# Optimization experiments

Measured on AMD Instinct MI355X. Metric: run time of the kernel, lower is better.

The kernel has to match this reference:

```python
import jax, jax.numpy as jnp
import numpy as np

H, W = 200, 200           # BEV spatial shape (single level)
NBQ, NH, NL, NP = 2, 8, 1, 4
D = 256
HD = D // NH


def setup_inputs() -> dict:
    key = jax.random.key(0)
    ks = jax.random.split(key, 12)
    bs, nq = 1, H * W
    query = jax.random.normal(ks[0], (bs, nq, D), jnp.float32)
    value = jax.random.normal(ks[1], (bs, NBQ * nq, D), jnp.float32)
    reference_points = jax.random.uniform(ks[2], (bs, nq, NL, 2), dtype=jnp.float32)
    spatial_shapes = jnp.array([[H, W]], dtype=jnp.int32)
    sc = 1.0 / np.sqrt(D)
    W_v = jax.random.normal(ks[3], (D, D), jnp.float32) * sc
    b_v = jax.random.normal(ks[4], (D,), jnp.float32) * 0.01
    W_so = jax.random.normal(ks[5], (2 * D, NBQ * NH * NL * NP * 2), jnp.float32) * 0.02
    b_so = jax.random.normal(ks[6], (NBQ * NH * NL * NP * 2,), jnp.float32) * 0.5
    W_aw = jax.random.normal(ks[7], (2 * D, NBQ * NH * NL * NP), jnp.float32) * 0.02
    b_aw = jax.random.normal(ks[8], (NBQ * NH * NL * NP,), jnp.float32) * 0.01
    W_o = jax.random.normal(ks[9], (D, D), jnp.float32) * sc
    b_o = jax.random.normal(ks[10], (D,), jnp.float32) * 0.01
    return {"query": query, "value": value, "reference_points": reference_points,
            "spatial_shapes": spatial_shapes,
            "W_v": W_v, "b_v": b_v, "W_so": W_so, "b_so": b_so,
            "W_aw": W_aw, "b_aw": b_aw, "W_o": W_o, "b_o": b_o}


def _ms_deform_attn(value, locs, attn):
    # value: (B, K, NH, HD); locs: (B, nq, NH, NL, NP, 2) in [0,1]; attn: (B, nq, NH, NL, NP)
    B, K, h, d = value.shape
    nq = locs.shape[1]
    out = jnp.zeros((B, nq, h, d), value.dtype)
    start = 0
    for l, (Hl, Wl) in enumerate([(H, W)]):
        v = value[:, start:start + Hl * Wl].transpose(0, 2, 1, 3).reshape(B * h, Hl * Wl, d)
        start += Hl * Wl
        g = locs[:, :, :, l]                      # (B, nq, h, NP, 2)
        # grid_sample(align_corners=False, padding='zeros') pixel coords
        x = g[..., 0] * Wl - 0.5
        y = g[..., 1] * Hl - 0.5
        x0 = jnp.floor(x); y0 = jnp.floor(y)
        lx = x - x0; ly = y - y0
        x0 = x0.astype(jnp.int32); y0 = y0.astype(jnp.int32)
        acc = jnp.zeros((B * h, nq * NP, d), value.dtype)
        for dy, wy in ((0, 1.0 - ly), (1, ly)):
            for dx, wx in ((0, 1.0 - lx), (1, lx)):
                xi = x0 + dx; yi = y0 + dy
                valid = ((xi >= 0) & (xi < Wl) & (yi >= 0) & (yi < Hl)).astype(value.dtype)
                idx = jnp.clip(yi, 0, Hl - 1) * Wl + jnp.clip(xi, 0, Wl - 1)  # (B,nq,h,NP)
                idxf = idx.transpose(0, 2, 1, 3).reshape(B * h, nq * NP)
                samp = jnp.take_along_axis(v, idxf[:, :, None], axis=1)       # (B*h, nq*NP, d)
                wgt = (wx * wy * valid).transpose(0, 2, 1, 3).reshape(B * h, nq * NP, 1)
                acc = acc + samp * wgt
        acc = acc.reshape(B, h, nq, NP, d)
        out = out + jnp.einsum('bhqpd,bqhp->bqhd', acc, attn[:, :, :, l])
    return out.reshape(B, nq, h * d)


def reference(query, value, reference_points, spatial_shapes,
              W_v, b_v, W_so, b_so, W_aw, b_aw, W_o, b_o):
    bs, nq, _ = query.shape
    identity = query
    val4 = value.reshape(bs, NBQ, nq, D)
    # query enhanced with most recent bev-queue features
    qe = jnp.concatenate([val4[:, 0], query], axis=-1)           # (bs, nq, 2D)
    vproj = (value @ W_v + b_v).reshape(bs * NBQ, nq, NH, HD)
    off = (qe @ W_so + b_so).reshape(bs, nq, NH, NBQ, NL, NP, 2)
    aw = (qe @ W_aw + b_aw).reshape(bs, nq, NH, NBQ, NL * NP)
    aw = jax.nn.softmax(aw, axis=-1).reshape(bs, nq, NH, NBQ, NL, NP)
    aw = aw.transpose(0, 3, 1, 2, 4, 5).reshape(bs * NBQ, nq, NH, NL, NP)
    # offset normalizer: [W, H] per level
    norm = jnp.stack([spatial_shapes[:, 1], spatial_shapes[:, 0]], -1).astype(query.dtype)  # (NL,2)
    locs = (reference_points[:, :, None, None, :, None, :]
            + off / norm[None, None, None, None, :, None, :])     # (bs,nq,NH,NBQ,NL,NP,2)
    locs = locs.transpose(0, 3, 1, 2, 4, 5, 6).reshape(bs * NBQ, nq, NH, NL, NP, 2)
    out = _ms_deform_attn(vproj, locs, aw)                        # (bs*NBQ, nq, D)
    out = out.reshape(bs, NBQ, nq, D).mean(axis=1)
    return out @ W_o + b_o + identity
```

## Files before the change

kernel.cpp:

```cpp
#include <hip/hip_runtime.h>
#include <math.h>

#define HW_   40000
#define NQ_   40000
#define IMGW  200
#define IMGH  200

typedef __bf16 bf16;
typedef __attribute__((ext_vector_type(4))) __bf16 bf16x4;
typedef __attribute__((ext_vector_type(8))) __bf16 bf16x8;
typedef __attribute__((ext_vector_type(4))) float f32x4;

__device__ __forceinline__ void gload_lds16(const void* g, void* l) {
  __builtin_amdgcn_global_load_lds(
      (const __attribute__((address_space(1))) void*)g,
      (__attribute__((address_space(3))) void*)l, 16, 0, 0);
}

__global__ __launch_bounds__(256) void prep_kernel(
    const float* __restrict__ Wv, const float* __restrict__ Wso,
    const float* __restrict__ Waw, const float* __restrict__ Wo,
    bf16* __restrict__ BtV, bf16* __restrict__ BtOA, bf16* __restrict__ BtO)
{
  int idx = blockIdx.x * 256 + threadIdx.x;
  if (idx < 65536) {
    int k = idx >> 8, n = idx & 255;
    BtV[(size_t)n * 256 + k] = (bf16)Wv[idx];
  } else if (idx < 131072) {
    int j = idx - 65536;
    int k = j >> 7, n = j & 127;
    BtOA[(size_t)n * 512 + k] = (bf16)Wso[j];
  } else if (idx < 163840) {
    int j = idx - 131072;
    int k = j >> 6, n = j & 63;
    BtOA[(size_t)(128 + n) * 512 + k] = (bf16)Waw[j];
  } else if (idx < 229376) {
    int j = idx - 163840;
    int k = j >> 8, n = j & 255;
    BtO[(size_t)n * 256 + k] = (bf16)Wo[j];
  }
}

template<int KT, int MODE, int BN, int AF32>
__global__ __launch_bounds__(256) void mfma_gemm_kernel(
    const void* __restrict__ A0, const void* __restrict__ A1,
    const bf16* __restrict__ Bt,
    const float* __restrict__ bias0, const float* __restrict__ bias1,
    const float* __restrict__ resid,
    void* __restrict__ outp, void* __restrict__ outp2, int M)
{
  constexpr int NT16 = BN / 32;
  constexpr int BCH  = BN / 64;
  __shared__ bf16 As[2][128 * 32];
  __shared__ bf16 Bs[2][BN * 32];
  const int t    = threadIdx.x;
  const int m0   = blockIdx.x * 128;
  const int w    = t >> 6;
  const int lane = t & 63;
  const int quad = lane >> 4;
  const int l16  = lane & 15;
  const int wm   = (w & 1) * 64;
  const int wn   = (w >> 1) * (BN / 2);

  f32x4 acc[4][NT16] = {};

  int gmA[2];
#pragma unroll
  for (int i = 0; i < 2; ++i) {
    int gm = m0 + ((i * 256 + t) >> 2);
    gmA[i] = (gm >= M) ? (M - 1) : gm;
  }

  float4 apf[2][2];

  auto issueB = [&](int it) {
    const int kt  = it * 32;
    const int buf = it & 1;
#pragma unroll
    for (int i = 0; i < BCH; ++i) {
      int c = i * 256 + t;
      gload_lds16(&Bt[(size_t)(c >> 2) * KT + kt + (c & 3) * 8], &Bs[buf][c * 8]);
    }
  };

  auto issueA_lds = [&](int it) {
    const int kt  = it * 32;
    const int buf = it & 1;
    const bf16* Ap;
    int col;
    if (KT == 512) { Ap = (kt < 256) ? (const bf16*)A0 : (const bf16*)A1; col = kt & 255; }
    else           { Ap = (const bf16*)A0; col = kt; }
#pragma unroll
    for (int i = 0; i < 2; ++i) {
      int c = i * 256 + t;
      gload_lds16(&Ap[(size_t)gmA[i] * 256 + col + (c & 3) * 8], &As[buf][c * 8]);
    }
  };

  auto loadA_f32 = [&](int it) {
    const int kt = it * 32;
    const float* Ap;
    int col;
    if (KT == 512) { Ap = (kt < 256) ? (const float*)A0 : (const float*)A1; col = kt & 255; }
    else           { Ap = (const float*)A0; col = kt; }
#pragma unroll
    for (int i = 0; i < 2; ++i) {
      int c = i * 256 + t;
      const float4* s = (const float4*)&Ap[(size_t)gmA[i] * 256 + col + (c & 3) * 8];
      apf[i][0] = s[0];
      apf[i][1] = s[1];
    }
  };

  auto writeA = [&](int it) {
    const int buf = it & 1;
#pragma unroll
    for (int i = 0; i < 2; ++i) {
      int c = i * 256 + t;
      bf16x8 o = {(bf16)apf[i][0].x, (bf16)apf[i][0].y,
                  (bf16)apf[i][0].z, (bf16)apf[i][0].w,
                  (bf16)apf[i][1].x, (bf16)apf[i][1].y,
                  (bf16)apf[i][1].z, (bf16)apf[i][1].w};
      *(bf16x8*)&As[buf][c * 8] = o;
    }
  };

  constexpr int NIT = KT / 32;
  if (AF32) { loadA_f32(0); issueB(0); writeA(0); }
  else      { issueA_lds(0); issueB(0); }

#pragma unroll
  for (int it = 0; it < NIT; ++it) {
    __syncthreads();
    if (it + 1 < NIT) {
      issueB(it + 1);
      if (AF32) loadA_f32(it + 1); else issueA_lds(it + 1);
    }
    const bf16* as = As[it & 1];
    const bf16* bs = Bs[it & 1];
    bf16x8 af[4], bfr[NT16];
#pragma unroll
    for (int x = 0; x < 4; ++x)
      af[x] = *(const bf16x8*)&as[(wm + x * 16 + l16) * 32 + quad * 8];
#pragma unroll
    for (int x = 0; x < NT16; ++x)
      bfr[x] = *(const bf16x8*)&bs[(wn + x * 16 + l16) * 32 + quad * 8];
#pragma unroll
    for (int mt = 0; mt < 4; ++mt)
#pragma unroll
      for (int nt = 0; nt < NT16; ++nt)
        acc[mt][nt] = __builtin_amdgcn_mfma_f32_16x16x32_bf16(
            af[mt], bfr[nt], acc[mt][nt], 0, 0, 0);
    if (AF32 && it + 1 < NIT) writeA(it + 1);
  }

#pragma unroll
  for (int mt = 0; mt < 4; ++mt) {
#pragma unroll
    for (int r = 0; r < 4; ++r) {
      const int gm = m0 + wm + mt * 16 + quad * 4 + r;
      if (gm >= M) continue;
#pragma unroll
      for (int nt = 0; nt < NT16; ++nt) {
        const int gn = wn + nt * 16 + l16;
        float v = acc[mt][nt][r];
        if (MODE == 0) {
          int nbq = (gm >= HW_) ? 1 : 0;
          int pix = gm - nbq * HW_;
          int h = gn >> 5, hd = gn & 31;
          ((bf16*)outp)[(((size_t)(nbq * 8 + h) * HW_ + pix) << 5) + hd] =
              (bf16)(v + bias0[gn]);
        } else if (MODE == 1) {
          if (gn < 128)
            ((bf16*)outp)[(size_t)gm * 128 + gn] = (bf16)(v + bias0[gn]);
          else
            ((bf16*)outp2)[(size_t)gm * 64 + (gn - 128)] =
                (bf16)(v + bias1[gn - 128]);
        } else {
          ((float*)outp)[(size_t)gm * 256 + gn] =
              v + bias0[gn] + resid[(size_t)gm * 256 + gn];
        }
      }
    }
  }
}

__global__ __launch_bounds__(256) void deform_attn_kernel(
    const bf16* __restrict__ vws,
    const bf16* __restrict__ off_bf,
    const bf16* __restrict__ aw_bf,
    const float* __restrict__ ref,
    bf16* __restrict__ ms)
{
  const int t    = threadIdx.x;
  const int w    = t >> 6;
  const int lane = t & 63;
  const int h    = blockIdx.x & 7;
  const int qb   = blockIdx.x >> 3;
  const int qi   = lane >> 3;
  const int q    = qb * 32 + w * 8 + qi;
  const int nbq  = (lane >> 2) & 1;
  const int sub  = lane & 3;
  const int g    = h * 2 + nbq;

  const float rx = ref[2 * q + 0] * (float)IMGW - 0.5f;
  const float ry = ref[2 * q + 1] * (float)IMGH - 0.5f;

  bf16x4 a4 = *(const bf16x4*)&aw_bf[(size_t)q * 64 + g * 4];
  float aa0 = (float)a4[0], aa1 = (float)a4[1], aa2 = (float)a4[2], aa3 = (float)a4[3];
  float mx = fmaxf(fmaxf(aa0, aa1), fmaxf(aa2, aa3));
  float e0 = __expf(aa0 - mx), e1 = __expf(aa1 - mx);
  float e2 = __expf(aa2 - mx), e3 = __expf(aa3 - mx);
  float inv = 1.0f / (e0 + e1 + e2 + e3);
  float w4[4] = {e0 * inv, e1 * inv, e2 * inv, e3 * inv};

  bf16x8 o8 = *(const bf16x8*)&off_bf[(size_t)q * 128 + g * 8];
  float ox[4] = {(float)o8[0], (float)o8[2], (float)o8[4], (float)o8[6]};
  float oy[4] = {(float)o8[1], (float)o8[3], (float)o8[5], (float)o8[7]};

  const bf16* vbase = vws + (((size_t)(nbq * 8 + h) * HW_) << 5) + sub * 8;

  float acc[8] = {};
#pragma unroll
  for (int p = 0; p < 4; ++p) {
    float x = rx + ox[p];
    float y = ry + oy[p];
    float xf = floorf(x), yf = floorf(y);
    int   x0 = (int)xf,   y0 = (int)yf;
    float lx = x - xf,    ly = y - yf;
    int   x1 = x0 + 1,    y1 = y0 + 1;
    float w00 = (1.0f - lx) * (1.0f - ly);
    float w01 = lx * (1.0f - ly);
    float w10 = (1.0f - lx) * ly;
    float w11 = lx * ly;
    if (x0 < 0 || x0 >= IMGW) { w00 = 0.0f; w10 = 0.0f; }
    if (x1 < 0 || x1 >= IMGW) { w01 = 0.0f; w11 = 0.0f; }
    if (y0 < 0 || y0 >= IMGH) { w00 = 0.0f; w01 = 0.0f; }
    if (y1 < 0 || y1 >= IMGH) { w10 = 0.0f; w11 = 0.0f; }
    int xc0 = min(max(x0, 0), IMGW - 1), xc1 = min(max(x1, 0), IMGW - 1);
    int yc0 = min(max(y0, 0), IMGH - 1), yc1 = min(max(y1, 0), IMGH - 1);
    bf16x8 v00 = *(const bf16x8*)&vbase[(size_t)(yc0 * IMGW + xc0) << 5];
    bf16x8 v01 = *(const bf16x8*)&vbase[(size_t)(yc0 * IMGW + xc1) << 5];
    bf16x8 v10 = *(const bf16x8*)&vbase[(size_t)(yc1 * IMGW + xc0) << 5];
    bf16x8 v11 = *(const bf16x8*)&vbase[(size_t)(yc1 * IMGW + xc1) << 5];
    float wp = w4[p];
#pragma unroll
    for (int j = 0; j < 8; ++j) {
      float s = w00 * (float)v00[j] + w01 * (float)v01[j] +
                w10 * (float)v10[j] + w11 * (float)v11[j];
      acc[j] = fmaf(wp, s, acc[j]);
    }
  }

#pragma unroll
  for (int j = 0; j < 8; ++j) acc[j] += __shfl_xor(acc[j], 4);

  if (nbq == 0) {
    bf16x8 o;
#pragma unroll
    for (int j = 0; j < 8; ++j) o[j] = (bf16)(0.5f * acc[j]);
    *(bf16x8*)&ms[(size_t)q * 256 + h * 32 + sub * 8] = o;
  }
}

extern "C" void kernel_launch(void* const* d_in, const int* in_sizes, int n_in,
                              void* d_out, int out_size, void* d_ws, size_t ws_size,
                              hipStream_t stream) {
  const float* query = (const float*)d_in[0];
  const float* value = (const float*)d_in[1];
  const float* ref   = (const float*)d_in[2];
  const float* Wv  = (const float*)d_in[4];
  const float* bv  = (const float*)d_in[5];
  const float* Wso = (const float*)d_in[6];
  const float* bso = (const float*)d_in[7];
  const float* Waw = (const float*)d_in[8];
  const float* baw = (const float*)d_in[9];
  const float* Wo  = (const float*)d_in[10];
  const float* bo  = (const float*)d_in[11];
  float* out = (float*)d_out;

  char* p = (char*)d_ws;
  bf16* vws    = (bf16*)p; p += (size_t)2 * 8 * HW_ * 32 * 2;
  bf16* off_bf = (bf16*)p; p += (size_t)NQ_ * 128 * 2;
  bf16* aw_bf  = (bf16*)p; p += (size_t)NQ_ * 64 * 2;
  bf16* ms     = (bf16*)p; p += (size_t)NQ_ * 256 * 2;
  bf16* BtV    = (bf16*)p; p += (size_t)256 * 256 * 2;
  bf16* BtOA   = (bf16*)p; p += (size_t)192 * 512 * 2;
  bf16* BtO    = (bf16*)p; p += (size_t)256 * 256 * 2;

  prep_kernel<<<896, 256, 0, stream>>>(Wv, Wso, Waw, Wo, BtV, BtOA, BtO);

  mfma_gemm_kernel<256, 0, 256, 1><<<625, 256, 0, stream>>>(
      value, nullptr, BtV, bv, nullptr, nullptr, vws, nullptr, 2 * HW_);
  mfma_gemm_kernel<512, 1, 192, 1><<<313, 256, 0, stream>>>(
      value, query, BtOA, bso, baw, nullptr, off_bf, aw_bf, NQ_);
  deform_attn_kernel<<<10000, 256, 0, stream>>>(vws, off_bf, aw_bf, ref, ms);
  mfma_gemm_kernel<256, 2, 256, 0><<<313, 256, 0, stream>>>(
      ms, nullptr, BtO, bo, nullptr, query, out, nullptr, NQ_);
}
```

Baseline: 305.6 us.

## Load GEMM fragments directly from global memory into registers, dropping LDS staging

The MFMA GEMM kernel no longer stages A and B tiles through double-buffered shared memory with async global-to-LDS loads and block barriers. Each wave now reads its own bf16x8 fragments straight from global memory into registers and prefetches the next K slice during compute. This removes the LDS traffic and the __syncthreads. In exchange, waves that share rows or columns fetch the same data redundantly and lean on the caches. For the bf16 A path, the next-slice loads are issued after the MFMAs, so there is little time to hide their latency.

After: 394.9 us. 29.2% more time.

```diff
diff --git a/kernel.cpp b/kernel.cpp
--- a/kernel.cpp
+++ b/kernel.cpp
@@ -10,12 +10,6 @@
 typedef __attribute__((ext_vector_type(4))) __bf16 bf16x4;
 typedef __attribute__((ext_vector_type(8))) __bf16 bf16x8;
 typedef __attribute__((ext_vector_type(4))) float f32x4;
-
-__device__ __forceinline__ void gload_lds16(const void* g, void* l) {
-  __builtin_amdgcn_global_load_lds(
-      (const __attribute__((address_space(1))) void*)g,
-      (__attribute__((address_space(3))) void*)l, 16, 0, 0);
-}
 
 __global__ __launch_bounds__(256) void prep_kernel(
     const float* __restrict__ Wv, const float* __restrict__ Wso,
@@ -50,9 +44,7 @@
     void* __restrict__ outp, void* __restrict__ outp2, int M)
 {
   constexpr int NT16 = BN / 32;
-  constexpr int BCH  = BN / 64;
-  __shared__ bf16 As[2][128 * 32];
-  __shared__ bf16 Bs[2][BN * 32];
+  constexpr int NIT  = KT / 32;
   const int t    = threadIdx.x;
   const int m0   = blockIdx.x * 128;
   const int w    = t >> 6;
@@ -64,94 +56,76 @@
 
   f32x4 acc[4][NT16] = {};
 
-  int gmA[2];
-#pragma unroll
-  for (int i = 0; i < 2; ++i) {
-    int gm = m0 + ((i * 256 + t) >> 2);
-    gmA[i] = (gm >= M) ? (M - 1) : gm;
-  }
-
-  float4 apf[2][2];
-
-  auto issueB = [&](int it) {
-    const int kt  = it * 32;
-    const int buf = it & 1;
-#pragma unroll
-    for (int i = 0; i < BCH; ++i) {
-      int c = i * 256 + t;
-      gload_lds16(&Bt[(size_t)(c >> 2) * KT + kt + (c & 3) * 8], &Bs[buf][c * 8]);
+  int aoff[4];
+#pragma unroll
+  for (int x = 0; x < 4; ++x) {
+    int r = m0 + wm + x * 16 + l16;
+    if (r >= M) r = M - 1;
+    aoff[x] = r * 256 + quad * 8;
+  }
+  int boff[NT16];
+#pragma unroll
+  for (int x = 0; x < NT16; ++x)
+    boff[x] = (wn + x * 16 + l16) * KT + quad * 8;
+
+  float4 a_f[4][2];
+  bf16x8 a_h[4];
+  bf16x8 b_r[NT16];
+
+  auto loadA = [&](int it) {
+    const int kt = it * 32;
+    if (AF32) {
+      const float* Ap; int col;
+      if (KT == 512) { Ap = (kt < 256) ? (const float*)A0 : (const float*)A1; col = kt & 255; }
+      else           { Ap = (const float*)A0; col = kt; }
+#pragma unroll
+      for (int x = 0; x < 4; ++x) {
+        const float4* s = (const float4*)&Ap[(size_t)(aoff[x] + col)];
+        a_f[x][0] = s[0];
+        a_f[x][1] = s[1];
+      }
+    } else {
+      const bf16* Ap = (const bf16*)A0;
+#pragma unroll
+      for (int x = 0; x < 4; ++x)
+        a_h[x] = *(const bf16x8*)&Ap[(size_t)aoff[x] + kt];
     }
   };
-
-  auto issueA_lds = [&](int it) {
-    const int kt  = it * 32;
-    const int buf = it & 1;
-    const bf16* Ap;
-    int col;
-    if (KT == 512) { Ap = (kt < 256) ? (const bf16*)A0 : (const bf16*)A1; col = kt & 255; }
-    else           { Ap = (const bf16*)A0; col = kt; }
-#pragma unroll
-    for (int i = 0; i < 2; ++i) {
-      int c = i * 256 + t;
-      gload_lds16(&Ap[(size_t)gmA[i] * 256 + col + (c & 3) * 8], &As[buf][c * 8]);
-    }
+  auto loadB = [&](int it) {
+    const int kt = it * 32;
+#pragma unroll
+    for (int x = 0; x < NT16; ++x)
+      b_r[x] = *(const bf16x8*)&Bt[(size_t)boff[x] + kt];
   };
 
-  auto loadA_f32 = [&](int it) {
-    const int kt = it * 32;
-    const float* Ap;
-    int col;
-    if (KT == 512) { Ap = (kt < 256) ? (const float*)A0 : (const float*)A1; col = kt & 255; }
-    else           { Ap = (const float*)A0; col = kt; }
-#pragma unroll
-    for (int i = 0; i < 2; ++i) {
-      int c = i * 256 + t;
-      const float4* s = (const float4*)&Ap[(size_t)gmA[i] * 256 + col + (c & 3) * 8];
-      apf[i][0] = s[0];
-      apf[i][1] = s[1];
-    }
-  };
-
-  auto writeA = [&](int it) {
-    const int buf = it & 1;
-#pragma unroll
-    for (int i = 0; i < 2; ++i) {
-      int c = i * 256 + t;
-      bf16x8 o = {(bf16)apf[i][0].x, (bf16)apf[i][0].y,
-                  (bf16)apf[i][0].z, (bf16)apf[i][0].w,
-                  (bf16)apf[i][1].x, (bf16)apf[i][1].y,
-                  (bf16)apf[i][1].z, (bf16)apf[i][1].w};
-      *(bf16x8*)&As[buf][c * 8] = o;
-    }
-  };
-
-  constexpr int NIT = KT / 32;
-  if (AF32) { loadA_f32(0); issueB(0); writeA(0); }
-  else      { issueA_lds(0); issueB(0); }
+  loadA(0);
+  loadB(0);
 
 #pragma unroll
   for (int it = 0; it < NIT; ++it) {
-    __syncthreads();
-    if (it + 1 < NIT) {
-      issueB(it + 1);
-      if (AF32) loadA_f32(it + 1); else issueA_lds(it + 1);
-    }
-    const bf16* as = As[it & 1];
-    const bf16* bs = Bs[it & 1];
-    bf16x8 af[4], bfr[NT16];
-#pragma unroll
-    for (int x = 0; x < 4; ++x)
-      af[x] = *(const bf16x8*)&as[(wm + x * 16 + l16) * 32 + quad * 8];
-#pragma unroll
-    for (int x = 0; x < NT16; ++x)
-      bfr[x] = *(const bf16x8*)&bs[(wn + x * 16 + l16) * 32 + quad * 8];
+    bf16x8 af[4];
+    if (AF32) {
+#pragma unroll
+      for (int x = 0; x < 4; ++x) {
+        float4 lo = a_f[x][0], hi = a_f[x][1];
+        af[x] = bf16x8{(bf16)lo.x, (bf16)lo.y, (bf16)lo.z, (bf16)lo.w,
+                       (bf16)hi.x, (bf16)hi.y, (bf16)hi.z, (bf16)hi.w};
+      }
+      if (it + 1 < NIT) loadA(it + 1);
+    } else {
+#pragma unroll
+      for (int x = 0; x < 4; ++x) af[x] = a_h[x];
+    }
 #pragma unroll
     for (int mt = 0; mt < 4; ++mt)
 #pragma unroll
       for (int nt = 0; nt < NT16; ++nt)
         acc[mt][nt] = __builtin_amdgcn_mfma_f32_16x16x32_bf16(
-            af[mt], bfr[nt], acc[mt][nt], 0, 0, 0);
-    if (AF32 && it + 1 < NIT) writeA(it + 1);
+            af[mt], b_r[nt], acc[mt][nt], 0, 0, 0);
+    if (it + 1 < NIT) {
+      if (!AF32) loadA(it + 1);
+      loadB(it + 1);
+    }
   }
 
 #pragma unroll
```

## Halve GEMM M-tile to 64 rows and XOR-swizzle LDS tiles

Applied to the files above, without the earlier changes.

The MFMA GEMM block tile shrinks from 128 to 64 rows, so each wave handles 32 rows, and all three GEMM launches double their grid size. The A and B shared-memory tiles now use an XOR swizzle on the 16-byte chunk index, keyed on row, to cut LDS bank conflicts on the fragment reads. The smaller tile gives more blocks and better occupancy on a 256-CU part. In exchange, each block reuses the B tile across fewer rows, so B traffic per output rises. The bf16 A path drops its KT==512 dual-pointer branch, which is safe only because that path is used just with KT=256.

After: 293.5 us. 4.0% less time.

```diff
diff --git a/kernel.cpp b/kernel.cpp
--- a/kernel.cpp
+++ b/kernel.cpp
@@ -51,81 +51,68 @@
 {
   constexpr int NT16 = BN / 32;
   constexpr int BCH  = BN / 64;
-  __shared__ bf16 As[2][128 * 32];
+  constexpr int NIT  = KT / 32;
+  __shared__ bf16 As[2][64 * 32];
   __shared__ bf16 Bs[2][BN * 32];
   const int t    = threadIdx.x;
-  const int m0   = blockIdx.x * 128;
+  const int m0   = blockIdx.x * 64;
   const int w    = t >> 6;
   const int lane = t & 63;
   const int quad = lane >> 4;
   const int l16  = lane & 15;
-  const int wm   = (w & 1) * 64;
+  const int wm   = (w & 1) * 32;
   const int wn   = (w >> 1) * (BN / 2);
 
-  f32x4 acc[4][NT16] = {};
-
-  int gmA[2];
-#pragma unroll
-  for (int i = 0; i < 2; ++i) {
-    int gm = m0 + ((i * 256 + t) >> 2);
-    gmA[i] = (gm >= M) ? (M - 1) : gm;
-  }
-
-  float4 apf[2][2];
+  f32x4 acc[2][NT16] = {};
+
+  int gmA;
+  {
+    int gm = m0 + (t >> 2);
+    gmA = (gm >= M) ? (M - 1) : gm;
+  }
+  const int arow = t >> 2;
+  const int akey = (arow >> 1) & 3;
+
+  float4 apf[2];
 
   auto issueB = [&](int it) {
     const int kt  = it * 32;
     const int buf = it & 1;
 #pragma unroll
     for (int i = 0; i < BCH; ++i) {
-      int c = i * 256 + t;
-      gload_lds16(&Bt[(size_t)(c >> 2) * KT + kt + (c & 3) * 8], &Bs[buf][c * 8]);
+      int c   = i * 256 + t;
+      int row = c >> 2;
+      int j   = (c & 3) ^ ((row >> 1) & 3);
+      gload_lds16(&Bt[(size_t)row * KT + kt + j * 8], &Bs[buf][c * 8]);
     }
   };
 
   auto issueA_lds = [&](int it) {
     const int kt  = it * 32;
     const int buf = it & 1;
-    const bf16* Ap;
-    int col;
-    if (KT == 512) { Ap = (kt < 256) ? (const bf16*)A0 : (const bf16*)A1; col = kt & 255; }
-    else           { Ap = (const bf16*)A0; col = kt; }
-#pragma unroll
-    for (int i = 0; i < 2; ++i) {
-      int c = i * 256 + t;
-      gload_lds16(&Ap[(size_t)gmA[i] * 256 + col + (c & 3) * 8], &As[buf][c * 8]);
-    }
+    const bf16* Ap = (const bf16*)A0;
+    int j = (t & 3) ^ akey;
+    gload_lds16(&Ap[(size_t)gmA * 256 + kt + j * 8], &As[buf][t * 8]);
   };
 
   auto loadA_f32 = [&](int it) {
     const int kt = it * 32;
-    const float* Ap;
-    int col;
+    const float* Ap; int col;
     if (KT == 512) { Ap = (kt < 256) ? (const float*)A0 : (const float*)A1; col = kt & 255; }
     else           { Ap = (const float*)A0; col = kt; }
-#pragma unroll
-    for (int i = 0; i < 2; ++i) {
-      int c = i * 256 + t;
-      const float4* s = (const float4*)&Ap[(size_t)gmA[i] * 256 + col + (c & 3) * 8];
-      apf[i][0] = s[0];
-      apf[i][1] = s[1];
-    }
+    const float4* s4 = (const float4*)&Ap[(size_t)gmA * 256 + col + (t & 3) * 8];
+    apf[0] = s4[0];
+    apf[1] = s4[1];
   };
 
   auto writeA = [&](int it) {
     const int buf = it & 1;
-#pragma unroll
-    for (int i = 0; i < 2; ++i) {
-      int c = i * 256 + t;
-      bf16x8 o = {(bf16)apf[i][0].x, (bf16)apf[i][0].y,
-                  (bf16)apf[i][0].z, (bf16)apf[i][0].w,
-                  (bf16)apf[i][1].x, (bf16)apf[i][1].y,
-                  (bf16)apf[i][1].z, (bf16)apf[i][1].w};
-      *(bf16x8*)&As[buf][c * 8] = o;
-    }
-  };
-
-  constexpr int NIT = KT / 32;
+    int j = (t & 3) ^ akey;
+    bf16x8 o = {(bf16)apf[0].x, (bf16)apf[0].y, (bf16)apf[0].z, (bf16)apf[0].w,
+                (bf16)apf[1].x, (bf16)apf[1].y, (bf16)apf[1].z, (bf16)apf[1].w};
+    *(bf16x8*)&As[buf][arow * 32 + j * 8] = o;
+  };
+
   if (AF32) { loadA_f32(0); issueB(0); writeA(0); }
   else      { issueA_lds(0); issueB(0); }
 
@@ -138,15 +125,19 @@
     }
     const bf16* as = As[it & 1];
     const bf16* bs = Bs[it & 1];
-    bf16x8 af[4], bfr[NT16];
-#pragma unroll
-    for (int x = 0; x < 4; ++x)
-      af[x] = *(const bf16x8*)&as[(wm + x * 16 + l16) * 32 + quad * 8];
-#pragma unroll
-    for (int x = 0; x < NT16; ++x)
-      bfr[x] = *(const bf16x8*)&bs[(wn + x * 16 + l16) * 32 + quad * 8];
-#pragma unroll
-    for (int mt = 0; mt < 4; ++mt)
+    bf16x8 af[2], bfr[NT16];
+#pragma unroll
+    for (int x = 0; x < 2; ++x) {
+      int row = wm + x * 16 + l16;
+      af[x] = *(const bf16x8*)&as[row * 32 + (quad ^ ((row >> 1) & 3)) * 8];
+    }
+#pragma unroll
+    for (int x = 0; x < NT16; ++x) {
+      int row = wn + x * 16 + l16;
+      bfr[x] = *(const bf16x8*)&bs[row * 32 + (quad ^ ((row >> 1) & 3)) * 8];
+    }
+#pragma unroll
+    for (int mt = 0; mt < 2; ++mt)
 #pragma unroll
       for (int nt = 0; nt < NT16; ++nt)
         acc[mt][nt] = __builtin_amdgcn_mfma_f32_16x16x32_bf16(
@@ -155,7 +146,7 @@
   }
 
 #pragma unroll
-  for (int mt = 0; mt < 4; ++mt) {
+  for (int mt = 0; mt < 2; ++mt) {
 #pragma unroll
     for (int r = 0; r < 4; ++r) {
       const int gm = m0 + wm + mt * 16 + quad * 4 + r;
@@ -290,11 +281,11 @@
 
   prep_kernel<<<896, 256, 0, stream>>>(Wv, Wso, Waw, Wo, BtV, BtOA, BtO);
 
-  mfma_gemm_kernel<256, 0, 256, 1><<<625, 256, 0, stream>>>(
+  mfma_gemm_kernel<256, 0, 256, 1><<<1250, 256, 0, stream>>>(
       value, nullptr, BtV, bv, nullptr, nullptr, vws, nullptr, 2 * HW_);
-  mfma_gemm_kernel<512, 1, 192, 1><<<313, 256, 0, stream>>>(
+  mfma_gemm_kernel<512, 1, 192, 1><<<625, 256, 0, stream>>>(
       value, query, BtOA, bso, baw, nullptr, off_bf, aw_bf, NQ_);
   deform_attn_kernel<<<10000, 256, 0, stream>>>(vws, off_bf, aw_bf, ref, ms);
-  mfma_gemm_kernel<256, 2, 256, 0><<<313, 256, 0, stream>>>(
+  mfma_gemm_kernel<256, 2, 256, 0><<<625, 256, 0, stream>>>(
       ms, nullptr, BtO, bo, nullptr, query, out, nullptr, NQ_);
 }
```
